# Kernel tuning notes

Measured on AMD Instinct MI355X. Metric: run time of the kernel, lower is better.

The kernel has to match this reference:

```python
import jax, jax.numpy as jnp
import numpy as np

N_NODES = 50000
IN_CH = 128
OUT_CH = 64
HEADS = 2
N_EDGES = 400000
NEG_SLOPE = 0.2  # PyG GATConv default


def _glorot(key, shape):
    fan_in, fan_out = shape[0], shape[-1]
    lim = jnp.sqrt(6.0 / (fan_in + fan_out))
    return jax.random.uniform(key, shape, jnp.float32, -lim, lim)


def setup_inputs() -> dict:
    key = jax.random.key(0)
    ks = jax.random.split(key, 12)
    hid = 2 * OUT_CH  # per-head channels of conv1
    inp = {
        "x": jax.random.normal(ks[0], (N_NODES, IN_CH), jnp.float32),
        "edge_index": jax.random.randint(ks[1], (2, N_EDGES), 0, N_NODES, jnp.int32),
        # conv1: in=IN_CH, out=hid per head, HEADS heads, concat
        "W1": _glorot(ks[2], (IN_CH, HEADS * hid)),
        "att_src1": _glorot(ks[3], (HEADS, hid)),
        "att_dst1": _glorot(ks[4], (HEADS, hid)),
        "b1": jnp.zeros((HEADS * hid,), jnp.float32),
        # conv_mu: in=hid*HEADS, out=OUT_CH, 1 head
        "W_mu": _glorot(ks[5], (hid * HEADS, OUT_CH)),
        "att_src_mu": _glorot(ks[6], (1, OUT_CH)),
        "att_dst_mu": _glorot(ks[7], (1, OUT_CH)),
        "b_mu": jnp.zeros((OUT_CH,), jnp.float32),
        # conv_logstd: same shapes as conv_mu
        "W_ls": _glorot(ks[8], (hid * HEADS, OUT_CH)),
        "att_src_ls": _glorot(ks[9], (1, OUT_CH)),
        "att_dst_ls": _glorot(ks[10], (1, OUT_CH)),
        "b_ls": jnp.zeros((OUT_CH,), jnp.float32),
    }
    return inp


def gat_conv(x, src, dst, W, att_src, att_dst, b, n_nodes):
    """PyG GATConv (add_self_loops handled by caller in src/dst)."""
    H, C = att_src.shape
    h = (x @ W).reshape(n_nodes, H, C)                       # [N,H,C]
    a_src = jnp.einsum('nhc,hc->nh', h, att_src)             # [N,H]
    a_dst = jnp.einsum('nhc,hc->nh', h, att_dst)
    e = jax.nn.leaky_relu(a_src[src] + a_dst[dst], NEG_SLOPE)  # [E,H]
    # scatter-softmax over incoming edges per destination node
    m = jax.ops.segment_max(e, dst, num_segments=n_nodes)
    e = jnp.exp(e - m[dst])
    denom = jax.ops.segment_sum(e, dst, num_segments=n_nodes)
    alpha = e / (denom[dst] + 1e-16)                          # [E,H]
    out = jax.ops.segment_sum(h[src] * alpha[:, :, None], dst,
                              num_segments=n_nodes)           # [N,H,C]
    return out.reshape(n_nodes, H * C) + b


def reference(x, edge_index, W1, att_src1, att_dst1, b1,
              W_mu, att_src_mu, att_dst_mu, b_mu,
              W_ls, att_src_ls, att_dst_ls, b_ls):
    n = x.shape[0]
    loop = jnp.arange(n, dtype=edge_index.dtype)
    src = jnp.concatenate([edge_index[0], loop])  # add self-loops (PyG default)
    dst = jnp.concatenate([edge_index[1], loop])
    h = jax.nn.elu(gat_conv(x, src, dst, W1, att_src1, att_dst1, b1, n))
    mu = gat_conv(h, src, dst, W_mu, att_src_mu, att_dst_mu, b_mu, n)
    logstd = gat_conv(h, src, dst, W_ls, att_src_ls, att_dst_ls, b_ls, n)
    return (mu, logstd)
```

## Files before the change

kernel.cpp:

```cpp
#include <hip/hip_runtime.h>
#include <math.h>

#define N_NODES 50000
#define N_EDGES 400000
#define PAD 64

typedef __attribute__((ext_vector_type(8))) short bf16x8;
typedef __attribute__((ext_vector_type(4))) float f32x4;

__device__ __forceinline__ float lrelu(float x){ return x > 0.f ? x : 0.2f*x; }
__device__ __forceinline__ float bf2f(unsigned short u){ return __uint_as_float(((unsigned int)u)<<16); }
__device__ __forceinline__ unsigned short f2bf(float f){
    unsigned int b = __float_as_uint(f);
    return (unsigned short)((b + 0x7FFFu + ((b>>16)&1u)) >> 16);
}
__device__ __forceinline__ float4 bf4(ushort4 u){
    return make_float4(bf2f(u.x), bf2f(u.y), bf2f(u.z), bf2f(u.w));
}
__device__ __forceinline__ float wexp(float e){ return __expf(fminf(e, 80.f)); }

__global__ __launch_bounds__(256) void prep_k(const float* __restrict__ x, unsigned short* __restrict__ xb,
        const float* __restrict__ W1, const float* __restrict__ Wmu, const float* __restrict__ Wls,
        unsigned short* __restrict__ W1T, unsigned short* __restrict__ WmlT,
        const int* __restrict__ src, const int* __restrict__ dst,
        int* __restrict__ counts, int* __restrict__ csr_src){
    int i = blockIdx.x*256 + threadIdx.x;
    if (i < (N_NODES*128)/4){
        float4 v = ((const float4*)x)[i];
        ((ushort4*)xb)[i] = make_ushort4(f2bf(v.x), f2bf(v.y), f2bf(v.z), f2bf(v.w));
    }
    if (i < 32768){
        int n = i >> 7, k = i & 127;
        W1T[i] = f2bf(W1[k*256 + n]);
        int n2 = i >> 8, k2 = i & 255;
        float v = (n2 < 64) ? Wmu[k2*64 + n2] : Wls[k2*64 + (n2-64)];
        WmlT[i] = f2bf(v);
    }
    if (i < N_EDGES){
        int d = dst[i];
        int pos = atomicAdd(&counts[d], 1);
        csr_src[d*PAD + pos] = src[i];
    }
}

template<int MODE>
__global__ __launch_bounds__(256) void mfma_gemm_k(const unsigned short* __restrict__ A,
        const unsigned short* __restrict__ BT, unsigned short* __restrict__ C,
        int M, int K, int ldc,
        const float* __restrict__ attS0, const float* __restrict__ attD0,
        const float* __restrict__ attS1, const float* __restrict__ attD1,
        float* __restrict__ outS, float* __restrict__ outD){
    __shared__ unsigned short As[128*40];
    __shared__ unsigned short Bs[128*40];
    int t = threadIdx.x;
    int lane = t & 63, wid = t >> 6;
    int wy = wid >> 1, wx = wid & 1;
    int quad = lane >> 4, l15 = lane & 15;
    int row0 = blockIdx.y * 128;
    int col0 = blockIdx.x * 128;

    f32x4 acc[4][4];
    #pragma unroll
    for (int i = 0; i < 4; i++)
        #pragma unroll
        for (int j = 0; j < 4; j++)
            acc[i][j] = (f32x4){0.f, 0.f, 0.f, 0.f};

    int r = t >> 2;
    int cofs = (t & 3) * 8;

    for (int k0 = 0; k0 < K; k0 += 32){
        int gr0 = min(row0 + r,      M-1);
        int gr1 = min(row0 + r + 64, M-1);
        float4 av0 = *(const float4*)(A  + (size_t)gr0*K + k0 + cofs);
        float4 av1 = *(const float4*)(A  + (size_t)gr1*K + k0 + cofs);
        float4 bv0 = *(const float4*)(BT + (size_t)(col0 + r)*K      + k0 + cofs);
        float4 bv1 = *(const float4*)(BT + (size_t)(col0 + r + 64)*K + k0 + cofs);
        __syncthreads();
        *(float4*)&As[r*40 + cofs]      = av0;
        *(float4*)&As[(r+64)*40 + cofs] = av1;
        *(float4*)&Bs[r*40 + cofs]      = bv0;
        *(float4*)&Bs[(r+64)*40 + cofs] = bv1;
        __syncthreads();

        bf16x8 af[4], bf[4];
        #pragma unroll
        for (int i = 0; i < 4; i++)
            af[i] = *(const bf16x8*)&As[(wy*64 + i*16 + l15)*40 + quad*8];
        #pragma unroll
        for (int j = 0; j < 4; j++)
            bf[j] = *(const bf16x8*)&Bs[(wx*64 + j*16 + l15)*40 + quad*8];
        #pragma unroll
        for (int i = 0; i < 4; i++)
            #pragma unroll
            for (int j = 0; j < 4; j++)
                acc[i][j] = __builtin_amdgcn_mfma_f32_16x16x32_bf16(af[i], bf[j], acc[i][j], 0, 0, 0);
    }

    int head = blockIdx.x;
    float aS[4], aD[4];
    #pragma unroll
    for (int j = 0; j < 4; j++){
        if (MODE == 1){
            int ch = wx*64 + j*16 + l15;
            aS[j] = attS0[head*128 + ch];
            aD[j] = attD0[head*128 + ch];
        } else {
            int c2 = j*16 + l15;
            aS[j] = wx ? attS1[c2] : attS0[c2];
            aD[j] = wx ? attD1[c2] : attD0[c2];
        }
    }

    #pragma unroll
    for (int i = 0; i < 4; i++){
        #pragma unroll
        for (int reg = 0; reg < 4; reg++){
            int rr = row0 + wy*64 + i*16 + quad*4 + reg;
            float sp = 0.f, dp = 0.f;
            #pragma unroll
            for (int j = 0; j < 4; j++){
                float v = acc[i][j][reg];
                int cc = col0 + wx*64 + j*16 + l15;
                if (rr < M) C[(size_t)rr*ldc + cc] = f2bf(v);
                sp = fmaf(v, aS[j], sp);
                dp = fmaf(v, aD[j], dp);
            }
            #pragma unroll
            for (int msk = 1; msk < 16; msk <<= 1){
                sp += __shfl_xor(sp, msk);
                dp += __shfl_xor(dp, msk);
            }
            if (l15 == 0 && rr < M){
                if (MODE == 1){
                    atomicAdd(&outS[rr*2 + head], sp);
                    atomicAdd(&outD[rr*2 + head], dp);
                } else {
                    outS[rr*2 + wx] = sp;
                    outD[rr*2 + wx] = dp;
                }
            }
        }
    }
}

__global__ __launch_bounds__(256) void agg1_k(const unsigned short* __restrict__ h1,
        const float* __restrict__ as, const float* __restrict__ ad,
        const int* __restrict__ counts, const int* __restrict__ csr_src,
        const float* __restrict__ b1, unsigned short* __restrict__ hout){
    int wave = threadIdx.x >> 6, lane = threadIdx.x & 63;
    int n = blockIdx.x*4 + wave;
    if (n >= N_NODES) return;
    int head = lane >> 5;
    const ushort4* h1v = (const ushort4*)h1;
    const float2* asv = (const float2*)as;

    float2 adn = ((const float2*)ad)[n], asn = asv[n];
    float adh = head ? adn.y : adn.x;
    float ash = head ? asn.y : asn.x;

    float w = wexp(lrelu(ash + adh));
    float l = w;
    float4 r = bf4(h1v[(size_t)n*64 + lane]);
    float4 acc = make_float4(w*r.x, w*r.y, w*r.z, w*r.w);

    int deg = counts[n];
    int off = n*PAD;
    int dm1 = deg - 1;
    for (int k = 0; k < deg; k += 4){
        int s0 = csr_src[off + k];
        int s1 = csr_src[off + min(k+1, dm1)];
        int s2 = csr_src[off + min(k+2, dm1)];
        int s3 = csr_src[off + min(k+3, dm1)];
        float2 a0 = asv[s0], a1 = asv[s1], a2 = asv[s2], a3 = asv[s3];
        float4 r0 = bf4(h1v[(size_t)s0*64 + lane]);
        float4 r1 = bf4(h1v[(size_t)s1*64 + lane]);
        float4 r2 = bf4(h1v[(size_t)s2*64 + lane]);
        float4 r3 = bf4(h1v[(size_t)s3*64 + lane]);
        float w0 = wexp(lrelu((head ? a0.y : a0.x) + adh));
        float w1 = (k+1 <= dm1) ? wexp(lrelu((head ? a1.y : a1.x) + adh)) : 0.f;
        float w2 = (k+2 <= dm1) ? wexp(lrelu((head ? a2.y : a2.x) + adh)) : 0.f;
        float w3 = (k+3 <= dm1) ? wexp(lrelu((head ? a3.y : a3.x) + adh)) : 0.f;
        l += (w0 + w1) + (w2 + w3);
        acc.x = fmaf(w0, r0.x, acc.x); acc.x = fmaf(w1, r1.x, acc.x);
        acc.x = fmaf(w2, r2.x, acc.x); acc.x = fmaf(w3, r3.x, acc.x);
        acc.y = fmaf(w0, r0.y, acc.y); acc.y = fmaf(w1, r1.y, acc.y);
        acc.y = fmaf(w2, r2.y, acc.y); acc.y = fmaf(w3, r3.y, acc.y);
        acc.z = fmaf(w0, r0.z, acc.z); acc.z = fmaf(w1, r1.z, acc.z);
        acc.z = fmaf(w2, r2.z, acc.z); acc.z = fmaf(w3, r3.z, acc.z);
        acc.w = fmaf(w0, r0.w, acc.w); acc.w = fmaf(w1, r1.w, acc.w);
        acc.w = fmaf(w2, r2.w, acc.w); acc.w = fmaf(w3, r3.w, acc.w);
    }

    float invl = 1.f / (l + 1e-16f);
    float4 b4 = *(const float4*)&b1[lane*4];
    float4 v;
    v.x = acc.x*invl + b4.x; v.y = acc.y*invl + b4.y;
    v.z = acc.z*invl + b4.z; v.w = acc.w*invl + b4.w;
    v.x = v.x > 0.f ? v.x : __expf(v.x) - 1.f;
    v.y = v.y > 0.f ? v.y : __expf(v.y) - 1.f;
    v.z = v.z > 0.f ? v.z : __expf(v.z) - 1.f;
    v.w = v.w > 0.f ? v.w : __expf(v.w) - 1.f;
    ((ushort4*)hout)[(size_t)n*64 + lane] = make_ushort4(f2bf(v.x), f2bf(v.y), f2bf(v.z), f2bf(v.w));
}

__global__ __launch_bounds__(256) void agg2_k(const unsigned short* __restrict__ hml,
        const float* __restrict__ as, const float* __restrict__ ad,
        const int* __restrict__ counts, const int* __restrict__ csr_src,
        const float* __restrict__ b_mu, const float* __restrict__ b_ls,
        float* __restrict__ out){
    int grp = threadIdx.x >> 5, lane = threadIdx.x & 31;
    int n = blockIdx.x*8 + grp;
    if (n >= N_NODES) return;
    int g = lane >> 4;
    const ushort4* hv = (const ushort4*)hml;
    const float2* asv = (const float2*)as;

    float2 adn = ((const float2*)ad)[n], asn = asv[n];
    float adh = g ? adn.y : adn.x;
    float ash = g ? asn.y : asn.x;

    float w = wexp(lrelu(ash + adh));
    float l = w;
    float4 r = bf4(hv[(size_t)n*32 + lane]);
    float4 acc = make_float4(w*r.x, w*r.y, w*r.z, w*r.w);

    int deg = counts[n];
    int off = n*PAD;
    int dm1 = deg - 1;
    for (int k = 0; k < deg; k += 4){
        int s0 = csr_src[off + k];
        int s1 = csr_src[off + min(k+1, dm1)];
        int s2 = csr_src[off + min(k+2, dm1)];
        int s3 = csr_src[off + min(k+3, dm1)];
        float2 a0 = asv[s0], a1 = asv[s1], a2 = asv[s2], a3 = asv[s3];
        float4 r0 = bf4(hv[(size_t)s0*32 + lane]);
        float4 r1 = bf4(hv[(size_t)s1*32 + lane]);
        float4 r2 = bf4(hv[(size_t)s2*32 + lane]);
        float4 r3 = bf4(hv[(size_t)s3*32 + lane]);
        float w0 = wexp(lrelu((g ? a0.y : a0.x) + adh));
        float w1 = (k+1 <= dm1) ? wexp(lrelu((g ? a1.y : a1.x) + adh)) : 0.f;
        float w2 = (k+2 <= dm1) ? wexp(lrelu((g ? a2.y : a2.x) + adh)) : 0.f;
        float w3 = (k+3 <= dm1) ? wexp(lrelu((g ? a3.y : a3.x) + adh)) : 0.f;
        l += (w0 + w1) + (w2 + w3);
        acc.x = fmaf(w0, r0.x, acc.x); acc.x = fmaf(w1, r1.x, acc.x);
        acc.x = fmaf(w2, r2.x, acc.x); acc.x = fmaf(w3, r3.x, acc.x);
        acc.y = fmaf(w0, r0.y, acc.y); acc.y = fmaf(w1, r1.y, acc.y);
        acc.y = fmaf(w2, r2.y, acc.y); acc.y = fmaf(w3, r3.y, acc.y);
        acc.z = fmaf(w0, r0.z, acc.z); acc.z = fmaf(w1, r1.z, acc.z);
        acc.z = fmaf(w2, r2.z, acc.z); acc.z = fmaf(w3, r3.z, acc.z);
        acc.w = fmaf(w0, r0.w, acc.w); acc.w = fmaf(w1, r1.w, acc.w);
        acc.w = fmaf(w2, r2.w, acc.w); acc.w = fmaf(w3, r3.w, acc.w);
    }

    float invl = 1.f / (l + 1e-16f);
    int c = (lane & 15) * 4;
    const float* bb = g ? b_ls : b_mu;
    float4 b4 = *(const float4*)&bb[c];
    float4 v;
    v.x = acc.x*invl + b4.x; v.y = acc.y*invl + b4.y;
    v.z = acc.z*invl + b4.z; v.w = acc.w*invl + b4.w;
    float* base = g ? (out + (size_t)N_NODES*64) : out;
    *(float4*)&base[(size_t)n*64 + c] = v;
}

extern "C" void kernel_launch(void* const* d_in, const int* in_sizes, int n_in,
                              void* d_out, int out_size, void* d_ws, size_t ws_size,
                              hipStream_t stream) {
    const float* x           = (const float*)d_in[0];
    const int*   ei          = (const int*)d_in[1];
    const float* W1          = (const float*)d_in[2];
    const float* att_src1    = (const float*)d_in[3];
    const float* att_dst1    = (const float*)d_in[4];
    const float* b1          = (const float*)d_in[5];
    const float* W_mu        = (const float*)d_in[6];
    const float* att_src_mu  = (const float*)d_in[7];
    const float* att_dst_mu  = (const float*)d_in[8];
    const float* b_mu        = (const float*)d_in[9];
    const float* W_ls        = (const float*)d_in[10];
    const float* att_src_ls  = (const float*)d_in[11];
    const float* att_dst_ls  = (const float*)d_in[12];
    const float* b_ls        = (const float*)d_in[13];
    float* out = (float*)d_out;

    const int* srcp = ei;
    const int* dstp = ei + N_EDGES;

    unsigned short* xb   = (unsigned short*)d_ws;
    unsigned short* h1   = xb   + (size_t)N_NODES*128;
    unsigned short* hbuf = h1   + (size_t)N_NODES*256;
    unsigned short* hml  = hbuf + (size_t)N_NODES*256;
    unsigned short* W1T  = hml  + (size_t)N_NODES*128;
    unsigned short* WmlT = W1T  + 32768;
    int*   counts = (int*)(WmlT + 32768);
    float* as1    = (float*)(counts + N_NODES);
    float* ad1    = as1 + 2*N_NODES;
    float* as2    = ad1 + 2*N_NODES;
    float* ad2    = as2 + 2*N_NODES;
    int*   csr    = (int*)(ad2 + 2*N_NODES);

    hipMemsetAsync(counts, 0, N_NODES*sizeof(int) + 4*N_NODES*sizeof(float), stream);

    prep_k<<<(N_NODES*128/4 + 255)/256, 256, 0, stream>>>(x, xb, W1, W_mu, W_ls, W1T, WmlT,
                                                          srcp, dstp, counts, csr);

    mfma_gemm_k<1><<<dim3(2, 391), 256, 0, stream>>>(xb, W1T, h1, N_NODES, 128, 256,
                                                     att_src1, att_dst1, nullptr, nullptr, as1, ad1);
    agg1_k<<<(N_NODES + 3) / 4, 256, 0, stream>>>(h1, as1, ad1, counts, csr, b1, hbuf);

    mfma_gemm_k<2><<<dim3(1, 391), 256, 0, stream>>>(hbuf, WmlT, hml, N_NODES, 256, 128,
                                                     att_src_mu, att_dst_mu, att_src_ls, att_dst_ls, as2, ad2);
    agg2_k<<<(N_NODES + 7) / 8, 256, 0, stream>>>(hml, as2, ad2, counts, csr, b_mu, b_ls, out);
}
```

Measured before the change: 234.7 us.

## Fuse all stages into one persistent cooperative kernel with grid syncs

Replaces the five separate launches (prep, two GEMMs, two aggregations) with a single cooperative persistent kernel that loops over tiles and node groups with grid-stride loops and separates stages with grid.sync(). The aim is to remove kernel launch overhead and inter-kernel gaps. In exchange, the grid is capped at 1024 blocks, giving less parallelism than the original launches for the aggregation phases. The kernel also pays for grid-wide barriers and may have worse occupancy from the combined register pressure under launch_bounds(256,4).

```diff
diff --git a/kernel.cpp b/kernel.cpp
--- a/kernel.cpp
+++ b/kernel.cpp
@@ -1,9 +1,16 @@
 #include <hip/hip_runtime.h>
+#include <hip/hip_cooperative_groups.h>
 #include <math.h>
+
+namespace cg = cooperative_groups;
 
 #define N_NODES 50000
 #define N_EDGES 400000
 #define PAD 64
+#define TILES1 782
+#define TILES2 391
+#define NG1 12500
+#define NG2 6250
 
 typedef __attribute__((ext_vector_type(8))) short bf16x8;
 typedef __attribute__((ext_vector_type(4))) float f32x4;
@@ -19,45 +26,19 @@
 }
 __device__ __forceinline__ float wexp(float e){ return __expf(fminf(e, 80.f)); }
 
-__global__ __launch_bounds__(256) void prep_k(const float* __restrict__ x, unsigned short* __restrict__ xb,
-        const float* __restrict__ W1, const float* __restrict__ Wmu, const float* __restrict__ Wls,
-        unsigned short* __restrict__ W1T, unsigned short* __restrict__ WmlT,
-        const int* __restrict__ src, const int* __restrict__ dst,
-        int* __restrict__ counts, int* __restrict__ csr_src){
-    int i = blockIdx.x*256 + threadIdx.x;
-    if (i < (N_NODES*128)/4){
-        float4 v = ((const float4*)x)[i];
-        ((ushort4*)xb)[i] = make_ushort4(f2bf(v.x), f2bf(v.y), f2bf(v.z), f2bf(v.w));
-    }
-    if (i < 32768){
-        int n = i >> 7, k = i & 127;
-        W1T[i] = f2bf(W1[k*256 + n]);
-        int n2 = i >> 8, k2 = i & 255;
-        float v = (n2 < 64) ? Wmu[k2*64 + n2] : Wls[k2*64 + (n2-64)];
-        WmlT[i] = f2bf(v);
-    }
-    if (i < N_EDGES){
-        int d = dst[i];
-        int pos = atomicAdd(&counts[d], 1);
-        csr_src[d*PAD + pos] = src[i];
-    }
-}
-
 template<int MODE>
-__global__ __launch_bounds__(256) void mfma_gemm_k(const unsigned short* __restrict__ A,
-        const unsigned short* __restrict__ BT, unsigned short* __restrict__ C,
-        int M, int K, int ldc,
+__device__ void gemm_tile(unsigned short* As, unsigned short* Bs,
+        const unsigned short* __restrict__ A, const unsigned short* __restrict__ BT,
+        unsigned short* __restrict__ C, int M, int K, int ldc, int bx, int by,
         const float* __restrict__ attS0, const float* __restrict__ attD0,
         const float* __restrict__ attS1, const float* __restrict__ attD1,
         float* __restrict__ outS, float* __restrict__ outD){
-    __shared__ unsigned short As[128*40];
-    __shared__ unsigned short Bs[128*40];
     int t = threadIdx.x;
     int lane = t & 63, wid = t >> 6;
     int wy = wid >> 1, wx = wid & 1;
     int quad = lane >> 4, l15 = lane & 15;
-    int row0 = blockIdx.y * 128;
-    int col0 = blockIdx.x * 128;
+    int row0 = by * 128;
+    int col0 = bx * 128;
 
     f32x4 acc[4][4];
     #pragma unroll
@@ -97,7 +78,7 @@
                 acc[i][j] = __builtin_amdgcn_mfma_f32_16x16x32_bf16(af[i], bf[j], acc[i][j], 0, 0, 0);
     }
 
-    int head = blockIdx.x;
+    int head = bx;
     float aS[4], aD[4];
     #pragma unroll
     for (int j = 0; j < 4; j++){
@@ -144,124 +125,167 @@
     }
 }
 
-__global__ __launch_bounds__(256) void agg1_k(const unsigned short* __restrict__ h1,
-        const float* __restrict__ as, const float* __restrict__ ad,
-        const int* __restrict__ counts, const int* __restrict__ csr_src,
-        const float* __restrict__ b1, unsigned short* __restrict__ hout){
-    int wave = threadIdx.x >> 6, lane = threadIdx.x & 63;
-    int n = blockIdx.x*4 + wave;
-    if (n >= N_NODES) return;
-    int head = lane >> 5;
-    const ushort4* h1v = (const ushort4*)h1;
-    const float2* asv = (const float2*)as;
-
-    float2 adn = ((const float2*)ad)[n], asn = asv[n];
-    float adh = head ? adn.y : adn.x;
-    float ash = head ? asn.y : asn.x;
-
-    float w = wexp(lrelu(ash + adh));
-    float l = w;
-    float4 r = bf4(h1v[(size_t)n*64 + lane]);
-    float4 acc = make_float4(w*r.x, w*r.y, w*r.z, w*r.w);
-
-    int deg = counts[n];
-    int off = n*PAD;
-    int dm1 = deg - 1;
-    for (int k = 0; k < deg; k += 4){
-        int s0 = csr_src[off + k];
-        int s1 = csr_src[off + min(k+1, dm1)];
-        int s2 = csr_src[off + min(k+2, dm1)];
-        int s3 = csr_src[off + min(k+3, dm1)];
-        float2 a0 = asv[s0], a1 = asv[s1], a2 = asv[s2], a3 = asv[s3];
-        float4 r0 = bf4(h1v[(size_t)s0*64 + lane]);
-        float4 r1 = bf4(h1v[(size_t)s1*64 + lane]);
-        float4 r2 = bf4(h1v[(size_t)s2*64 + lane]);
-        float4 r3 = bf4(h1v[(size_t)s3*64 + lane]);
-        float w0 = wexp(lrelu((head ? a0.y : a0.x) + adh));
-        float w1 = (k+1 <= dm1) ? wexp(lrelu((head ? a1.y : a1.x) + adh)) : 0.f;
-        float w2 = (k+2 <= dm1) ? wexp(lrelu((head ? a2.y : a2.x) + adh)) : 0.f;
-        float w3 = (k+3 <= dm1) ? wexp(lrelu((head ? a3.y : a3.x) + adh)) : 0.f;
-        l += (w0 + w1) + (w2 + w3);
-        acc.x = fmaf(w0, r0.x, acc.x); acc.x = fmaf(w1, r1.x, acc.x);
-        acc.x = fmaf(w2, r2.x, acc.x); acc.x = fmaf(w3, r3.x, acc.x);
-        acc.y = fmaf(w0, r0.y, acc.y); acc.y = fmaf(w1, r1.y, acc.y);
-        acc.y = fmaf(w2, r2.y, acc.y); acc.y = fmaf(w3, r3.y, acc.y);
-        acc.z = fmaf(w0, r0.z, acc.z); acc.z = fmaf(w1, r1.z, acc.z);
-        acc.z = fmaf(w2, r2.z, acc.z); acc.z = fmaf(w3, r3.z, acc.z);
-        acc.w = fmaf(w0, r0.w, acc.w); acc.w = fmaf(w1, r1.w, acc.w);
-        acc.w = fmaf(w2, r2.w, acc.w); acc.w = fmaf(w3, r3.w, acc.w);
-    }
-
-    float invl = 1.f / (l + 1e-16f);
-    float4 b4 = *(const float4*)&b1[lane*4];
-    float4 v;
-    v.x = acc.x*invl + b4.x; v.y = acc.y*invl + b4.y;
-    v.z = acc.z*invl + b4.z; v.w = acc.w*invl + b4.w;
-    v.x = v.x > 0.f ? v.x : __expf(v.x) - 1.f;
-    v.y = v.y > 0.f ? v.y : __expf(v.y) - 1.f;
-    v.z = v.z > 0.f ? v.z : __expf(v.z) - 1.f;
-    v.w = v.w > 0.f ? v.w : __expf(v.w) - 1.f;
-    ((ushort4*)hout)[(size_t)n*64 + lane] = make_ushort4(f2bf(v.x), f2bf(v.y), f2bf(v.z), f2bf(v.w));
-}
-
-__global__ __launch_bounds__(256) void agg2_k(const unsigned short* __restrict__ hml,
-        const float* __restrict__ as, const float* __restrict__ ad,
-        const int* __restrict__ counts, const int* __restrict__ csr_src,
-        const float* __restrict__ b_mu, const float* __restrict__ b_ls,
-        float* __restrict__ out){
-    int grp = threadIdx.x >> 5, lane = threadIdx.x & 31;
-    int n = blockIdx.x*8 + grp;
-    if (n >= N_NODES) return;
-    int g = lane >> 4;
-    const ushort4* hv = (const ushort4*)hml;
-    const float2* asv = (const float2*)as;
-
-    float2 adn = ((const float2*)ad)[n], asn = asv[n];
-    float adh = g ? adn.y : adn.x;
-    float ash = g ? asn.y : asn.x;
-
-    float w = wexp(lrelu(ash + adh));
-    float l = w;
-    float4 r = bf4(hv[(size_t)n*32 + lane]);
-    float4 acc = make_float4(w*r.x, w*r.y, w*r.z, w*r.w);
-
-    int deg = counts[n];
-    int off = n*PAD;
-    int dm1 = deg - 1;
-    for (int k = 0; k < deg; k += 4){
-        int s0 = csr_src[off + k];
-        int s1 = csr_src[off + min(k+1, dm1)];
-        int s2 = csr_src[off + min(k+2, dm1)];
-        int s3 = csr_src[off + min(k+3, dm1)];
-        float2 a0 = asv[s0], a1 = asv[s1], a2 = asv[s2], a3 = asv[s3];
-        float4 r0 = bf4(hv[(size_t)s0*32 + lane]);
-        float4 r1 = bf4(hv[(size_t)s1*32 + lane]);
-        float4 r2 = bf4(hv[(size_t)s2*32 + lane]);
-        float4 r3 = bf4(hv[(size_t)s3*32 + lane]);
-        float w0 = wexp(lrelu((g ? a0.y : a0.x) + adh));
-        float w1 = (k+1 <= dm1) ? wexp(lrelu((g ? a1.y : a1.x) + adh)) : 0.f;
-        float w2 = (k+2 <= dm1) ? wexp(lrelu((g ? a2.y : a2.x) + adh)) : 0.f;
-        float w3 = (k+3 <= dm1) ? wexp(lrelu((g ? a3.y : a3.x) + adh)) : 0.f;
-        l += (w0 + w1) + (w2 + w3);
-        acc.x = fmaf(w0, r0.x, acc.x); acc.x = fmaf(w1, r1.x, acc.x);
-        acc.x = fmaf(w2, r2.x, acc.x); acc.x = fmaf(w3, r3.x, acc.x);
-        acc.y = fmaf(w0, r0.y, acc.y); acc.y = fmaf(w1, r1.y, acc.y);
-        acc.y = fmaf(w2, r2.y, acc.y); acc.y = fmaf(w3, r3.y, acc.y);
-        acc.z = fmaf(w0, r0.z, acc.z); acc.z = fmaf(w1, r1.z, acc.z);
-        acc.z = fmaf(w2, r2.z, acc.z); acc.z = fmaf(w3, r3.z, acc.z);
-        acc.w = fmaf(w0, r0.w, acc.w); acc.w = fmaf(w1, r1.w, acc.w);
-        acc.w = fmaf(w2, r2.w, acc.w); acc.w = fmaf(w3, r3.w, acc.w);
-    }
-
-    float invl = 1.f / (l + 1e-16f);
-    int c = (lane & 15) * 4;
-    const float* bb = g ? b_ls : b_mu;
-    float4 b4 = *(const float4*)&bb[c];
-    float4 v;
-    v.x = acc.x*invl + b4.x; v.y = acc.y*invl + b4.y;
-    v.z = acc.z*invl + b4.z; v.w = acc.w*invl + b4.w;
-    float* base = g ? (out + (size_t)N_NODES*64) : out;
-    *(float4*)&base[(size_t)n*64 + c] = v;
+__global__ __launch_bounds__(256, 4) void fused_k(
+        const float* __restrict__ x, const int* __restrict__ src, const int* __restrict__ dst,
+        const float* __restrict__ W1, const float* __restrict__ attS1v, const float* __restrict__ attD1v,
+        const float* __restrict__ b1,
+        const float* __restrict__ Wmu, const float* __restrict__ attSmu, const float* __restrict__ attDmu,
+        const float* __restrict__ bmu,
+        const float* __restrict__ Wls, const float* __restrict__ attSls, const float* __restrict__ attDls,
+        const float* __restrict__ bls,
+        unsigned short* __restrict__ xb, unsigned short* __restrict__ h1,
+        unsigned short* __restrict__ hbuf, unsigned short* __restrict__ hml,
+        unsigned short* __restrict__ W1T, unsigned short* __restrict__ WmlT,
+        int* __restrict__ counts, int* __restrict__ csr,
+        float* __restrict__ as1, float* __restrict__ ad1,
+        float* __restrict__ as2, float* __restrict__ ad2,
+        float* __restrict__ out)
+{
+    __shared__ unsigned short As[128*40];
+    __shared__ unsigned short Bs[128*40];
+    cg::grid_group grid = cg::this_grid();
+    const int tid = threadIdx.x, bid = blockIdx.x, nb = gridDim.x;
+    const int gthr = bid*256 + tid, gsz = nb*256;
+
+    for (int i = gthr; i < (N_NODES*128)/4; i += gsz){
+        float4 v = ((const float4*)x)[i];
+        ((ushort4*)xb)[i] = make_ushort4(f2bf(v.x), f2bf(v.y), f2bf(v.z), f2bf(v.w));
+    }
+    for (int i = gthr; i < 32768; i += gsz){
+        int n = i >> 7, k = i & 127;
+        W1T[i] = f2bf(W1[k*256 + n]);
+        int n2 = i >> 8, k2 = i & 255;
+        float v = (n2 < 64) ? Wmu[k2*64 + n2] : Wls[k2*64 + (n2-64)];
+        WmlT[i] = f2bf(v);
+    }
+    for (int e = gthr; e < N_EDGES; e += gsz){
+        int d = dst[e];
+        int pos = atomicAdd(&counts[d], 1);
+        csr[d*PAD + pos] = src[e];
+    }
+    grid.sync();
+
+    for (int t = bid; t < TILES1; t += nb)
+        gemm_tile<1>(As, Bs, xb, W1T, h1, N_NODES, 128, 256, t & 1, t >> 1,
+                     attS1v, attD1v, nullptr, nullptr, as1, ad1);
+    grid.sync();
+
+    for (int g = bid; g < NG1; g += nb){
+        int wave = tid >> 6, lane = tid & 63;
+        int n = g*4 + wave;
+        int head = lane >> 5;
+        const ushort4* h1v = (const ushort4*)h1;
+        const float2* asv = (const float2*)as1;
+
+        float2 adn = ((const float2*)ad1)[n], asn = asv[n];
+        float adh = head ? adn.y : adn.x;
+        float ash = head ? asn.y : asn.x;
+
+        float w = wexp(lrelu(ash + adh));
+        float l = w;
+        float4 r = bf4(h1v[(size_t)n*64 + lane]);
+        float4 acc = make_float4(w*r.x, w*r.y, w*r.z, w*r.w);
+
+        int deg = counts[n];
+        int off = n*PAD;
+        int dm1 = deg - 1;
+        for (int k = 0; k < deg; k += 4){
+            int s0 = csr[off + k];
+            int s1 = csr[off + min(k+1, dm1)];
+            int s2 = csr[off + min(k+2, dm1)];
+            int s3 = csr[off + min(k+3, dm1)];
+            float2 a0 = asv[s0], a1 = asv[s1], a2 = asv[s2], a3 = asv[s3];
+            float4 r0 = bf4(h1v[(size_t)s0*64 + lane]);
+            float4 r1 = bf4(h1v[(size_t)s1*64 + lane]);
+            float4 r2 = bf4(h1v[(size_t)s2*64 + lane]);
+            float4 r3 = bf4(h1v[(size_t)s3*64 + lane]);
+            float w0 = wexp(lrelu((head ? a0.y : a0.x) + adh));
+            float w1 = (k+1 <= dm1) ? wexp(lrelu((head ? a1.y : a1.x) + adh)) : 0.f;
+            float w2 = (k+2 <= dm1) ? wexp(lrelu((head ? a2.y : a2.x) + adh)) : 0.f;
+            float w3 = (k+3 <= dm1) ? wexp(lrelu((head ? a3.y : a3.x) + adh)) : 0.f;
+            l += (w0 + w1) + (w2 + w3);
+            acc.x = fmaf(w0, r0.x, acc.x); acc.x = fmaf(w1, r1.x, acc.x);
+            acc.x = fmaf(w2, r2.x, acc.x); acc.x = fmaf(w3, r3.x, acc.x);
+            acc.y = fmaf(w0, r0.y, acc.y); acc.y = fmaf(w1, r1.y, acc.y);
+            acc.y = fmaf(w2, r2.y, acc.y); acc.y = fmaf(w3, r3.y, acc.y);
+            acc.z = fmaf(w0, r0.z, acc.z); acc.z = fmaf(w1, r1.z, acc.z);
+            acc.z = fmaf(w2, r2.z, acc.z); acc.z = fmaf(w3, r3.z, acc.z);
+            acc.w = fmaf(w0, r0.w, acc.w); acc.w = fmaf(w1, r1.w, acc.w);
+            acc.w = fmaf(w2, r2.w, acc.w); acc.w = fmaf(w3, r3.w, acc.w);
+        }
+
+        float invl = 1.f / (l + 1e-16f);
+        float4 b4 = *(const float4*)&b1[lane*4];
+        float4 v;
+        v.x = acc.x*invl + b4.x; v.y = acc.y*invl + b4.y;
+        v.z = acc.z*invl + b4.z; v.w = acc.w*invl + b4.w;
+        v.x = v.x > 0.f ? v.x : __expf(v.x) - 1.f;
+        v.y = v.y > 0.f ? v.y : __expf(v.y) - 1.f;
+        v.z = v.z > 0.f ? v.z : __expf(v.z) - 1.f;
+        v.w = v.w > 0.f ? v.w : __expf(v.w) - 1.f;
+        ((ushort4*)hbuf)[(size_t)n*64 + lane] = make_ushort4(f2bf(v.x), f2bf(v.y), f2bf(v.z), f2bf(v.w));
+    }
+    grid.sync();
+
+    for (int t = bid; t < TILES2; t += nb)
+        gemm_tile<2>(As, Bs, hbuf, WmlT, hml, N_NODES, 256, 128, 0, t,
+                     attSmu, attDmu, attSls, attDls, as2, ad2);
+    grid.sync();
+
+    for (int g = bid; g < NG2; g += nb){
+        int grp = tid >> 5, lane = tid & 31;
+        int n = g*8 + grp;
+        int gg = lane >> 4;
+        const ushort4* hv = (const ushort4*)hml;
+        const float2* asv = (const float2*)as2;
+
+        float2 adn = ((const float2*)ad2)[n], asn = asv[n];
+        float adh = gg ? adn.y : adn.x;
+        float ash = gg ? asn.y : asn.x;
+
+        float w = wexp(lrelu(ash + adh));
+        float l = w;
+        float4 r = bf4(hv[(size_t)n*32 + lane]);
+        float4 acc = make_float4(w*r.x, w*r.y, w*r.z, w*r.w);
+
+        int deg = counts[n];
+        int off = n*PAD;
+        int dm1 = deg - 1;
+        for (int k = 0; k < deg; k += 4){
+            int s0 = csr[off + k];
+            int s1 = csr[off + min(k+1, dm1)];
+            int s2 = csr[off + min(k+2, dm1)];
+            int s3 = csr[off + min(k+3, dm1)];
+            float2 a0 = asv[s0], a1 = asv[s1], a2 = asv[s2], a3 = asv[s3];
+            float4 r0 = bf4(hv[(size_t)s0*32 + lane]);
+            float4 r1 = bf4(hv[(size_t)s1*32 + lane]);
+            float4 r2 = bf4(hv[(size_t)s2*32 + lane]);
+            float4 r3 = bf4(hv[(size_t)s3*32 + lane]);
+            float w0 = wexp(lrelu((gg ? a0.y : a0.x) + adh));
+            float w1 = (k+1 <= dm1) ? wexp(lrelu((gg ? a1.y : a1.x) + adh)) : 0.f;
+            float w2 = (k+2 <= dm1) ? wexp(lrelu((gg ? a2.y : a2.x) + adh)) : 0.f;
+            float w3 = (k+3 <= dm1) ? wexp(lrelu((gg ? a3.y : a3.x) + adh)) : 0.f;
+            l += (w0 + w1) + (w2 + w3);
+            acc.x = fmaf(w0, r0.x, acc.x); acc.x = fmaf(w1, r1.x, acc.x);
+            acc.x = fmaf(w2, r2.x, acc.x); acc.x = fmaf(w3, r3.x, acc.x);
+            acc.y = fmaf(w0, r0.y, acc.y); acc.y = fmaf(w1, r1.y, acc.y);
+            acc.y = fmaf(w2, r2.y, acc.y); acc.y = fmaf(w3, r3.y, acc.y);
+            acc.z = fmaf(w0, r0.z, acc.z); acc.z = fmaf(w1, r1.z, acc.z);
+            acc.z = fmaf(w2, r2.z, acc.z); acc.z = fmaf(w3, r3.z, acc.z);
+            acc.w = fmaf(w0, r0.w, acc.w); acc.w = fmaf(w1, r1.w, acc.w);
+            acc.w = fmaf(w2, r2.w, acc.w); acc.w = fmaf(w3, r3.w, acc.w);
+        }
+
+        float invl = 1.f / (l + 1e-16f);
+        int c = (lane & 15) * 4;
+        const float* bb = gg ? bls : bmu;
+        float4 b4 = *(const float4*)&bb[c];
+        float4 v;
+        v.x = acc.x*invl + b4.x; v.y = acc.y*invl + b4.y;
+        v.z = acc.z*invl + b4.z; v.w = acc.w*invl + b4.w;
+        float* base = gg ? (out + (size_t)N_NODES*64) : out;
+        *(float4*)&base[(size_t)n*64 + c] = v;
+    }
 }
 
 extern "C" void kernel_launch(void* const* d_in, const int* in_sizes, int n_in,
@@ -301,14 +325,22 @@
 
     hipMemsetAsync(counts, 0, N_NODES*sizeof(int) + 4*N_NODES*sizeof(float), stream);
 
-    prep_k<<<(N_NODES*128/4 + 255)/256, 256, 0, stream>>>(x, xb, W1, W_mu, W_ls, W1T, WmlT,
-                                                          srcp, dstp, counts, csr);
-
-    mfma_gemm_k<1><<<dim3(2, 391), 256, 0, stream>>>(xb, W1T, h1, N_NODES, 128, 256,
-                                                     att_src1, att_dst1, nullptr, nullptr, as1, ad1);
-    agg1_k<<<(N_NODES + 3) / 4, 256, 0, stream>>>(h1, as1, ad1, counts, csr, b1, hbuf);
-
-    mfma_gemm_k<2><<<dim3(1, 391), 256, 0, stream>>>(hbuf, WmlT, hml, N_NODES, 256, 128,
-                                                     att_src_mu, att_dst_mu, att_src_ls, att_dst_ls, as2, ad2);
-    agg2_k<<<(N_NODES + 7) / 8, 256, 0, stream>>>(hml, as2, ad2, counts, csr, b_mu, b_ls, out);
-}
+    int occ = 0;
+    if (hipOccupancyMaxActiveBlocksPerMultiprocessor(&occ, (const void*)fused_k, 256, 0) != hipSuccess || occ < 1)
+        occ = 1;
+    int grid = occ * 256;
+    if (grid > 1024) grid = 1024;
+
+    void* args[] = {
+        (void*)&x, (void*)&srcp, (void*)&dstp,
+        (void*)&W1, (void*)&att_src1, (void*)&att_dst1, (void*)&b1,
+        (void*)&W_mu, (void*)&att_src_mu, (void*)&att_dst_mu, (void*)&b_mu,
+        (void*)&W_ls, (void*)&att_src_ls, (void*)&att_dst_ls, (void*)&b_ls,
+        (void*)&xb, (void*)&h1, (void*)&hbuf, (void*)&hml,
+        (void*)&W1T, (void*)&WmlT,
+        (void*)&counts, (void*)&csr,
+        (void*)&as1, (void*)&ad1, (void*)&as2, (void*)&ad2,
+        (void*)&out
+    };
+    hipLaunchCooperativeKernel((const void*)fused_k, dim3(grid), dim3(256), args, 0, stream);
+}
```

Measured after the change: 562.4 us. 2.4x slower.

## Aggregate raw features before layer-1 GEMM using precomputed attention projections

Applied to the files above, without the earlier changes.

Layer 1 is reordered from transform-then-aggregate to aggregate-then-transform. Per-node attention logits now come from x dotted with a precomputed W1·att vector, built by a new single-block kernel and applied inside the prep kernel. Each head's softmax-weighted sum of 128-wide bf16 input rows is then fed to the GEMM, which also applies bias and ELU, removing the separate 256-wide h1 gather and the atomic logit epilogue. The cost is two 128-wide aggregate buffers in place of one 256-wide one, plus an extra small kernel launch. Bias is now added outside the aggregation, which is exact only because the softmax weights sum to one.

```diff
diff --git a/kernel.cpp b/kernel.cpp
--- a/kernel.cpp
+++ b/kernel.cpp
@@ -19,34 +19,136 @@
 }
 __device__ __forceinline__ float wexp(float e){ return __expf(fminf(e, 80.f)); }
 
+__global__ __launch_bounds__(256) void vprep_k(const float* __restrict__ W1,
+        const float* __restrict__ attS, const float* __restrict__ attD,
+        float* __restrict__ V1){
+    int t = threadIdx.x;
+    for (int idx = t; idx < 512; idx += 256){
+        int v = idx >> 7, k = idx & 127;
+        int h = v & 1;
+        const float* attp = (v >> 1) ? attD : attS;
+        float s = 0.f;
+        #pragma unroll 8
+        for (int c = 0; c < 128; c++)
+            s = fmaf(W1[k*256 + h*128 + c], attp[h*128 + c], s);
+        V1[idx] = s;
+    }
+}
+
 __global__ __launch_bounds__(256) void prep_k(const float* __restrict__ x, unsigned short* __restrict__ xb,
+        const float* __restrict__ V1, float2* __restrict__ as1, float2* __restrict__ ad1,
         const float* __restrict__ W1, const float* __restrict__ Wmu, const float* __restrict__ Wls,
         unsigned short* __restrict__ W1T, unsigned short* __restrict__ WmlT,
         const int* __restrict__ src, const int* __restrict__ dst,
         int* __restrict__ counts, int* __restrict__ csr_src){
-    int i = blockIdx.x*256 + threadIdx.x;
-    if (i < (N_NODES*128)/4){
-        float4 v = ((const float4*)x)[i];
-        ((ushort4*)xb)[i] = make_ushort4(f2bf(v.x), f2bf(v.y), f2bf(v.z), f2bf(v.w));
-    }
-    if (i < 32768){
-        int n = i >> 7, k = i & 127;
-        W1T[i] = f2bf(W1[k*256 + n]);
+    int t = threadIdx.x;
+    int gthr = blockIdx.x*256 + t;
+
+    int n = blockIdx.x*4 + (t >> 6);
+    int lane = t & 63;
+    if (n < N_NODES){
+        int c0 = lane*2;
+        float2 xv = ((const float2*)(x + (size_t)n*128))[lane];
+        ((ushort2*)(xb + (size_t)n*128))[lane] = make_ushort2(f2bf(xv.x), f2bf(xv.y));
+        float s0 = xv.x*V1[      c0] + xv.y*V1[      c0+1];
+        float s1 = xv.x*V1[128 + c0] + xv.y*V1[128 + c0+1];
+        float d0 = xv.x*V1[256 + c0] + xv.y*V1[256 + c0+1];
+        float d1 = xv.x*V1[384 + c0] + xv.y*V1[384 + c0+1];
+        #pragma unroll
+        for (int m = 1; m < 64; m <<= 1){
+            s0 += __shfl_xor(s0, m);
+            s1 += __shfl_xor(s1, m);
+            d0 += __shfl_xor(d0, m);
+            d1 += __shfl_xor(d1, m);
+        }
+        if (lane == 0){
+            as1[n] = make_float2(s0, s1);
+            ad1[n] = make_float2(d0, d1);
+        }
+    }
+
+    if (gthr < 32768){
+        int i = gthr;
+        int nn = i >> 7, k = i & 127;
+        W1T[i] = f2bf(W1[k*256 + nn]);
         int n2 = i >> 8, k2 = i & 255;
         float v = (n2 < 64) ? Wmu[k2*64 + n2] : Wls[k2*64 + (n2-64)];
         WmlT[i] = f2bf(v);
     }
-    if (i < N_EDGES){
-        int d = dst[i];
+
+    if (gthr < N_EDGES){
+        int d = dst[gthr];
         int pos = atomicAdd(&counts[d], 1);
-        csr_src[d*PAD + pos] = src[i];
-    }
+        csr_src[d*PAD + pos] = src[gthr];
+    }
+}
+
+__global__ __launch_bounds__(256) void agg1x_k(const unsigned short* __restrict__ xb,
+        const float2* __restrict__ as, const float2* __restrict__ ad,
+        const int* __restrict__ counts, const int* __restrict__ csr_src,
+        unsigned short* __restrict__ aggx0, unsigned short* __restrict__ aggx1){
+    int wave = threadIdx.x >> 6, lane = threadIdx.x & 63;
+    int n = blockIdx.x*4 + wave;
+    if (n >= N_NODES) return;
+
+    float2 adn = ad[n], asn = as[n];
+    float w0s = wexp(lrelu(asn.x + adn.x));
+    float w1s = wexp(lrelu(asn.y + adn.y));
+    float l0 = w0s, l1 = w1s;
+
+    ushort2 u = ((const ushort2*)(xb + (size_t)n*128))[lane];
+    float rx = bf2f(u.x), ry = bf2f(u.y);
+    float a0x = w0s*rx, a0y = w0s*ry;
+    float a1x = w1s*rx, a1y = w1s*ry;
+
+    int deg = counts[n];
+    int off = n*PAD;
+    int dm1 = deg - 1;
+    for (int k = 0; k < deg; k += 4){
+        int s0 = csr_src[off + k];
+        int s1 = csr_src[off + min(k+1, dm1)];
+        int s2 = csr_src[off + min(k+2, dm1)];
+        int s3 = csr_src[off + min(k+3, dm1)];
+        float2 e0 = as[s0], e1 = as[s1], e2 = as[s2], e3 = as[s3];
+        ushort2 u0 = ((const ushort2*)(xb + (size_t)s0*128))[lane];
+        ushort2 u1 = ((const ushort2*)(xb + (size_t)s1*128))[lane];
+        ushort2 u2 = ((const ushort2*)(xb + (size_t)s2*128))[lane];
+        ushort2 u3 = ((const ushort2*)(xb + (size_t)s3*128))[lane];
+        float w00 = wexp(lrelu(e0.x + adn.x));
+        float w01 = wexp(lrelu(e0.y + adn.y));
+        float w10 = (k+1 <= dm1) ? wexp(lrelu(e1.x + adn.x)) : 0.f;
+        float w11 = (k+1 <= dm1) ? wexp(lrelu(e1.y + adn.y)) : 0.f;
+        float w20 = (k+2 <= dm1) ? wexp(lrelu(e2.x + adn.x)) : 0.f;
+        float w21 = (k+2 <= dm1) ? wexp(lrelu(e2.y + adn.y)) : 0.f;
+        float w30 = (k+3 <= dm1) ? wexp(lrelu(e3.x + adn.x)) : 0.f;
+        float w31 = (k+3 <= dm1) ? wexp(lrelu(e3.y + adn.y)) : 0.f;
+        l0 += (w00 + w10) + (w20 + w30);
+        l1 += (w01 + w11) + (w21 + w31);
+        float r0x = bf2f(u0.x), r0y = bf2f(u0.y);
+        float r1x = bf2f(u1.x), r1y = bf2f(u1.y);
+        float r2x = bf2f(u2.x), r2y = bf2f(u2.y);
+        float r3x = bf2f(u3.x), r3y = bf2f(u3.y);
+        a0x = fmaf(w00, r0x, a0x); a0y = fmaf(w00, r0y, a0y);
+        a1x = fmaf(w01, r0x, a1x); a1y = fmaf(w01, r0y, a1y);
+        a0x = fmaf(w10, r1x, a0x); a0y = fmaf(w10, r1y, a0y);
+        a1x = fmaf(w11, r1x, a1x); a1y = fmaf(w11, r1y, a1y);
+        a0x = fmaf(w20, r2x, a0x); a0y = fmaf(w20, r2y, a0y);
+        a1x = fmaf(w21, r2x, a1x); a1y = fmaf(w21, r2y, a1y);
+        a0x = fmaf(w30, r3x, a0x); a0y = fmaf(w30, r3y, a0y);
+        a1x = fmaf(w31, r3x, a1x); a1y = fmaf(w31, r3y, a1y);
+    }
+
+    float i0 = 1.f / (l0 + 1e-16f);
+    float i1 = 1.f / (l1 + 1e-16f);
+    ((ushort2*)(aggx0 + (size_t)n*128))[lane] = make_ushort2(f2bf(a0x*i0), f2bf(a0y*i0));
+    ((ushort2*)(aggx1 + (size_t)n*128))[lane] = make_ushort2(f2bf(a1x*i1), f2bf(a1y*i1));
 }
 
 template<int MODE>
-__global__ __launch_bounds__(256) void mfma_gemm_k(const unsigned short* __restrict__ A,
+__global__ __launch_bounds__(256) void mfma_gemm_k(const unsigned short* __restrict__ A0,
+        const unsigned short* __restrict__ A1,
         const unsigned short* __restrict__ BT, unsigned short* __restrict__ C,
-        int M, int K, int ldc,
+        int M, int K, int ldc, const float* __restrict__ bias,
         const float* __restrict__ attS0, const float* __restrict__ attD0,
         const float* __restrict__ attS1, const float* __restrict__ attD1,
         float* __restrict__ outS, float* __restrict__ outD){
@@ -58,6 +160,7 @@
     int quad = lane >> 4, l15 = lane & 15;
     int row0 = blockIdx.y * 128;
     int col0 = blockIdx.x * 128;
+    const unsigned short* A = (MODE == 0 && blockIdx.x) ? A1 : A0;
 
     f32x4 acc[4][4];
     #pragma unroll
@@ -97,14 +200,12 @@
                 acc[i][j] = __builtin_amdgcn_mfma_f32_16x16x32_bf16(af[i], bf[j], acc[i][j], 0, 0, 0);
     }
 
-    int head = blockIdx.x;
-    float aS[4], aD[4];
+    float aS[4], aD[4], bvals[4];
     #pragma unroll
     for (int j = 0; j < 4; j++){
-        if (MODE == 1){
-            int ch = wx*64 + j*16 + l15;
-            aS[j] = attS0[head*128 + ch];
-            aD[j] = attD0[head*128 + ch];
+        int cc = col0 + wx*64 + j*16 + l15;
+        if (MODE == 0){
+            bvals[j] = bias[cc];
         } else {
             int c2 = j*16 + l15;
             aS[j] = wx ? attS1[c2] : attS0[c2];
@@ -117,91 +218,38 @@
         #pragma unroll
         for (int reg = 0; reg < 4; reg++){
             int rr = row0 + wy*64 + i*16 + quad*4 + reg;
-            float sp = 0.f, dp = 0.f;
-            #pragma unroll
-            for (int j = 0; j < 4; j++){
-                float v = acc[i][j][reg];
-                int cc = col0 + wx*64 + j*16 + l15;
-                if (rr < M) C[(size_t)rr*ldc + cc] = f2bf(v);
-                sp = fmaf(v, aS[j], sp);
-                dp = fmaf(v, aD[j], dp);
-            }
-            #pragma unroll
-            for (int msk = 1; msk < 16; msk <<= 1){
-                sp += __shfl_xor(sp, msk);
-                dp += __shfl_xor(dp, msk);
-            }
-            if (l15 == 0 && rr < M){
-                if (MODE == 1){
-                    atomicAdd(&outS[rr*2 + head], sp);
-                    atomicAdd(&outD[rr*2 + head], dp);
-                } else {
+            if (MODE == 0){
+                if (rr < M){
+                    #pragma unroll
+                    for (int j = 0; j < 4; j++){
+                        int cc = col0 + wx*64 + j*16 + l15;
+                        float v = acc[i][j][reg] + bvals[j];
+                        v = v > 0.f ? v : __expf(v) - 1.f;
+                        C[(size_t)rr*ldc + cc] = f2bf(v);
+                    }
+                }
+            } else {
+                float sp = 0.f, dp = 0.f;
+                #pragma unroll
+                for (int j = 0; j < 4; j++){
+                    float v = acc[i][j][reg];
+                    int cc = col0 + wx*64 + j*16 + l15;
+                    if (rr < M) C[(size_t)rr*ldc + cc] = f2bf(v);
+                    sp = fmaf(v, aS[j], sp);
+                    dp = fmaf(v, aD[j], dp);
+                }
+                #pragma unroll
+                for (int msk = 1; msk < 16; msk <<= 1){
+                    sp += __shfl_xor(sp, msk);
+                    dp += __shfl_xor(dp, msk);
+                }
+                if (l15 == 0 && rr < M){
                     outS[rr*2 + wx] = sp;
                     outD[rr*2 + wx] = dp;
                 }
             }
         }
     }
-}
-
-__global__ __launch_bounds__(256) void agg1_k(const unsigned short* __restrict__ h1,
-        const float* __restrict__ as, const float* __restrict__ ad,
-        const int* __restrict__ counts, const int* __restrict__ csr_src,
-        const float* __restrict__ b1, unsigned short* __restrict__ hout){
-    int wave = threadIdx.x >> 6, lane = threadIdx.x & 63;
-    int n = blockIdx.x*4 + wave;
-    if (n >= N_NODES) return;
-    int head = lane >> 5;
-    const ushort4* h1v = (const ushort4*)h1;
-    const float2* asv = (const float2*)as;
-
-    float2 adn = ((const float2*)ad)[n], asn = asv[n];
-    float adh = head ? adn.y : adn.x;
-    float ash = head ? asn.y : asn.x;
-
-    float w = wexp(lrelu(ash + adh));
-    float l = w;
-    float4 r = bf4(h1v[(size_t)n*64 + lane]);
-    float4 acc = make_float4(w*r.x, w*r.y, w*r.z, w*r.w);
-
-    int deg = counts[n];
-    int off = n*PAD;
-    int dm1 = deg - 1;
-    for (int k = 0; k < deg; k += 4){
-        int s0 = csr_src[off + k];
-        int s1 = csr_src[off + min(k+1, dm1)];
-        int s2 = csr_src[off + min(k+2, dm1)];
-        int s3 = csr_src[off + min(k+3, dm1)];
-        float2 a0 = asv[s0], a1 = asv[s1], a2 = asv[s2], a3 = asv[s3];
-        float4 r0 = bf4(h1v[(size_t)s0*64 + lane]);
-        float4 r1 = bf4(h1v[(size_t)s1*64 + lane]);
-        float4 r2 = bf4(h1v[(size_t)s2*64 + lane]);
-        float4 r3 = bf4(h1v[(size_t)s3*64 + lane]);
-        float w0 = wexp(lrelu((head ? a0.y : a0.x) + adh));
-        float w1 = (k+1 <= dm1) ? wexp(lrelu((head ? a1.y : a1.x) + adh)) : 0.f;
-        float w2 = (k+2 <= dm1) ? wexp(lrelu((head ? a2.y : a2.x) + adh)) : 0.f;
-        float w3 = (k+3 <= dm1) ? wexp(lrelu((head ? a3.y : a3.x) + adh)) : 0.f;
-        l += (w0 + w1) + (w2 + w3);
-        acc.x = fmaf(w0, r0.x, acc.x); acc.x = fmaf(w1, r1.x, acc.x);
-        acc.x = fmaf(w2, r2.x, acc.x); acc.x = fmaf(w3, r3.x, acc.x);
-        acc.y = fmaf(w0, r0.y, acc.y); acc.y = fmaf(w1, r1.y, acc.y);
-        acc.y = fmaf(w2, r2.y, acc.y); acc.y = fmaf(w3, r3.y, acc.y);
-        acc.z = fmaf(w0, r0.z, acc.z); acc.z = fmaf(w1, r1.z, acc.z);
-        acc.z = fmaf(w2, r2.z, acc.z); acc.z = fmaf(w3, r3.z, acc.z);
-        acc.w = fmaf(w0, r0.w, acc.w); acc.w = fmaf(w1, r1.w, acc.w);
-        acc.w = fmaf(w2, r2.w, acc.w); acc.w = fmaf(w3, r3.w, acc.w);
-    }
-
-    float invl = 1.f / (l + 1e-16f);
-    float4 b4 = *(const float4*)&b1[lane*4];
-    float4 v;
-    v.x = acc.x*invl + b4.x; v.y = acc.y*invl + b4.y;
-    v.z = acc.z*invl + b4.z; v.w = acc.w*invl + b4.w;
-    v.x = v.x > 0.f ? v.x : __expf(v.x) - 1.f;
-    v.y = v.y > 0.f ? v.y : __expf(v.y) - 1.f;
-    v.z = v.z > 0.f ? v.z : __expf(v.z) - 1.f;
-    v.w = v.w > 0.f ? v.w : __expf(v.w) - 1.f;
-    ((ushort4*)hout)[(size_t)n*64 + lane] = make_ushort4(f2bf(v.x), f2bf(v.y), f2bf(v.z), f2bf(v.w));
 }
 
 __global__ __launch_bounds__(256) void agg2_k(const unsigned short* __restrict__ hml,
@@ -214,11 +262,9 @@
     if (n >= N_NODES) return;
     int g = lane >> 4;
     const ushort4* hv = (const ushort4*)hml;
-    const float2* asv = (const float2*)as;
-
-    float2 adn = ((const float2*)ad)[n], asn = asv[n];
-    float adh = g ? adn.y : adn.x;
-    float ash = g ? asn.y : asn.x;
+
+    float adh = ad[n*2 + g];
+    float ash = as[n*2 + g];
 
     float w = wexp(lrelu(ash + adh));
     float l = w;
@@ -233,15 +279,16 @@
         int s1 = csr_src[off + min(k+1, dm1)];
         int s2 = csr_src[off + min(k+2, dm1)];
         int s3 = csr_src[off + min(k+3, dm1)];
-        float2 a0 = asv[s0], a1 = asv[s1], a2 = asv[s2], a3 = asv[s3];
+        float e0 = as[s0*2 + g], e1 = as[s1*2 + g];
+        float e2 = as[s2*2 + g], e3 = as[s3*2 + g];
         float4 r0 = bf4(hv[(size_t)s0*32 + lane]);
         float4 r1 = bf4(hv[(size_t)s1*32 + lane]);
         float4 r2 = bf4(hv[(size_t)s2*32 + lane]);
         float4 r3 = bf4(hv[(size_t)s3*32 + lane]);
-        float w0 = wexp(lrelu((g ? a0.y : a0.x) + adh));
-        float w1 = (k+1 <= dm1) ? wexp(lrelu((g ? a1.y : a1.x) + adh)) : 0.f;
-        float w2 = (k+2 <= dm1) ? wexp(lrelu((g ? a2.y : a2.x) + adh)) : 0.f;
-        float w3 = (k+3 <= dm1) ? wexp(lrelu((g ? a3.y : a3.x) + adh)) : 0.f;
+        float w0 = wexp(lrelu(e0 + adh));
+        float w1 = (k+1 <= dm1) ? wexp(lrelu(e1 + adh)) : 0.f;
+        float w2 = (k+2 <= dm1) ? wexp(lrelu(e2 + adh)) : 0.f;
+        float w3 = (k+3 <= dm1) ? wexp(lrelu(e3 + adh)) : 0.f;
         l += (w0 + w1) + (w2 + w3);
         acc.x = fmaf(w0, r0.x, acc.x); acc.x = fmaf(w1, r1.x, acc.x);
         acc.x = fmaf(w2, r2.x, acc.x); acc.x = fmaf(w3, r3.x, acc.x);
@@ -286,29 +333,37 @@
     const int* srcp = ei;
     const int* dstp = ei + N_EDGES;
 
-    unsigned short* xb   = (unsigned short*)d_ws;
-    unsigned short* h1   = xb   + (size_t)N_NODES*128;
-    unsigned short* hbuf = h1   + (size_t)N_NODES*256;
-    unsigned short* hml  = hbuf + (size_t)N_NODES*256;
-    unsigned short* W1T  = hml  + (size_t)N_NODES*128;
-    unsigned short* WmlT = W1T  + 32768;
+    unsigned short* xb    = (unsigned short*)d_ws;
+    unsigned short* aggx0 = xb    + (size_t)N_NODES*128;
+    unsigned short* aggx1 = aggx0 + (size_t)N_NODES*128;
+    unsigned short* hbuf  = aggx1 + (size_t)N_NODES*128;
+    unsigned short* hml   = hbuf  + (size_t)N_NODES*256;
+    unsigned short* W1T   = hml   + (size_t)N_NODES*128;
+    unsigned short* WmlT  = W1T   + 32768;
     int*   counts = (int*)(WmlT + 32768);
-    float* as1    = (float*)(counts + N_NODES);
-    float* ad1    = as1 + 2*N_NODES;
-    float* as2    = ad1 + 2*N_NODES;
-    float* ad2    = as2 + 2*N_NODES;
-    int*   csr    = (int*)(ad2 + 2*N_NODES);
-
-    hipMemsetAsync(counts, 0, N_NODES*sizeof(int) + 4*N_NODES*sizeof(float), stream);
-
-    prep_k<<<(N_NODES*128/4 + 255)/256, 256, 0, stream>>>(x, xb, W1, W_mu, W_ls, W1T, WmlT,
-                                                          srcp, dstp, counts, csr);
-
-    mfma_gemm_k<1><<<dim3(2, 391), 256, 0, stream>>>(xb, W1T, h1, N_NODES, 128, 256,
-                                                     att_src1, att_dst1, nullptr, nullptr, as1, ad1);
-    agg1_k<<<(N_NODES + 3) / 4, 256, 0, stream>>>(h1, as1, ad1, counts, csr, b1, hbuf);
-
-    mfma_gemm_k<2><<<dim3(1, 391), 256, 0, stream>>>(hbuf, WmlT, hml, N_NODES, 256, 128,
-                                                     att_src_mu, att_dst_mu, att_src_ls, att_dst_ls, as2, ad2);
+    float2* as1   = (float2*)(counts + N_NODES);
+    float2* ad1   = as1 + N_NODES;
+    float*  as2   = (float*)(ad1 + N_NODES);
+    float*  ad2   = as2 + 2*N_NODES;
+    float*  V1    = ad2 + 2*N_NODES;
+    int*    csr   = (int*)(V1 + 512);
+
+    hipMemsetAsync(counts, 0, N_NODES*sizeof(int), stream);
+
+    vprep_k<<<1, 256, 0, stream>>>(W1, att_src1, att_dst1, V1);
+
+    prep_k<<<12500, 256, 0, stream>>>(x, xb, V1, as1, ad1, W1, W_mu, W_ls, W1T, WmlT,
+                                      srcp, dstp, counts, csr);
+
+    agg1x_k<<<(N_NODES + 3) / 4, 256, 0, stream>>>(xb, as1, ad1, counts, csr, aggx0, aggx1);
+
+    mfma_gemm_k<0><<<dim3(2, 391), 256, 0, stream>>>(aggx0, aggx1, W1T, hbuf, N_NODES, 128, 256,
+                                                     b1, nullptr, nullptr, nullptr, nullptr,
+                                                     nullptr, nullptr);
+
+    mfma_gemm_k<2><<<dim3(1, 391), 256, 0, stream>>>(hbuf, hbuf, WmlT, hml, N_NODES, 256, 128,
+                                                     nullptr, att_src_mu, att_dst_mu,
+                                                     att_src_ls, att_dst_ls, as2, ad2);
+
     agg2_k<<<(N_NODES + 7) / 8, 256, 0, stream>>>(hml, as2, ad2, counts, csr, b_mu, b_ls, out);
 }
```

Result: no change. 231.4 us (-1.4%).
